# Kernel tuning notes

Measured on AMD Instinct MI355X. Metric: run time of the kernel, lower is better.

## Reference

```python
import jax, jax.numpy as jnp
import numpy as np

DIM = 768
HEADS = 12
HEAD_DIM = DIM // HEADS
SCALE = HEAD_DIM ** -0.5
BATCH = 4      # B videos
FRAMES = 64    # f frames
NTOK = 128     # W_TP tokens per window


def setup_inputs() -> dict:
    key = jax.random.key(0)
    ks = jax.random.split(key, 6)
    x = jax.random.normal(ks[0], (BATCH * FRAMES, NTOK, DIM), jnp.float32)
    # binary mask per frame (zeros are later masked_fill'd to -10000)
    mask = (jax.random.uniform(ks[1], (FRAMES, NTOK, NTOK)) > 0.2).astype(jnp.float32)
    edge_bias = jax.random.normal(ks[2], (NTOK, NTOK), jnp.float32)
    qkv_w = jax.random.normal(ks[3], (3 * DIM, DIM), jnp.float32) * (DIM ** -0.5)
    qkv_b = jnp.zeros((3 * DIM,), jnp.float32)
    proj_w = jax.random.normal(ks[4], (DIM, DIM), jnp.float32) * (DIM ** -0.5)
    proj_b = jnp.zeros((DIM,), jnp.float32)
    return {"x": x, "mask": mask, "edge_bias": edge_bias,
            "qkv_w": qkv_w, "qkv_b": qkv_b,
            "proj_w": proj_w, "proj_b": proj_b,
            "B": BATCH, "f": FRAMES}


def reference(x, mask, edge_bias, qkv_w, qkv_b, proj_w, proj_b, B, f):
    B_f, N, D = x.shape
    H, Dh = HEADS, D // HEADS
    # qkv projection -> [3, B_f, H, N, Dh]
    qkv = (x @ qkv_w.T + qkv_b).reshape(B_f, N, 3, H, Dh)
    qkv = jnp.transpose(qkv, (2, 0, 3, 1, 4))
    q = qkv[0] * jnp.float32(SCALE)
    k = qkv[1]
    v = qkv[2]
    # raw scores [B_f, H, N, N]
    attn = jnp.einsum('bhnd,bhmd->bhnm', q, k)
    # mask multiply ([1,f,1,N,N]) and edge-bias multiply ([1,1,1,N,N])
    attn = attn.reshape(B, f, H, N, N)
    attn = attn * mask[None, :, None] * edge_bias[None, None, None]
    attn = attn.reshape(B_f, H, N, N)
    # masked_fill(attn == 0, -10000) then softmax of NEGATED scores
    attn = jnp.where(attn == 0.0, jnp.float32(-10000.0), attn)
    attn = jax.nn.softmax(-attn, axis=-1)
    out = jnp.einsum('bhnm,bhmd->bhnd', attn, v)  # [B_f,H,N,Dh]
    out = jnp.transpose(out, (0, 2, 1, 3)).reshape(B_f, N, D)
    return out @ proj_w.T + proj_b
```

## Files before the change

kernel.cpp:

```cpp
#include <hip/hip_runtime.h>

typedef unsigned short u16;
typedef unsigned int   u32;
typedef unsigned long long u64;

typedef __attribute__((ext_vector_type(8))) short bf16x8;
typedef __attribute__((ext_vector_type(4))) float f32x4;
typedef __attribute__((ext_vector_type(4))) unsigned int u32x4;

__device__ __forceinline__ u16 rne_bf16(float f) {
  u32 u = __builtin_bit_cast(u32, f);
  u = (u + 0x7fffu + ((u >> 16) & 1u)) >> 16;
  return (u16)u;
}
__device__ __forceinline__ u32 pack_bf16x2(float lo, float hi) {
  return (u32)rne_bf16(lo) | ((u32)rne_bf16(hi) << 16);
}
__device__ __forceinline__ u32 cvt_pk_bf16(float lo, float hi) {
  u32 r;
  asm volatile("v_cvt_pk_bf16_f32 %0, %1, %2" : "=v"(r) : "v"(lo), "v"(hi));
  return r;
}

__global__ __launch_bounds__(256)
void prep_small(const float* __restrict__ mask,
                const float* __restrict__ proj_w, const float* __restrict__ qkv_b,
                const float* __restrict__ proj_b,
                u64* __restrict__ bm0, u64* __restrict__ bm1,
                float* __restrict__ invc, float* __restrict__ cbias) {
  const int b = blockIdx.x;
  const int lane = threadIdx.x & 63;
  if (b < 2048) {
    int row = b * 4 + (threadIdx.x >> 6);
    float v0 = mask[(long)row * 128 + lane];
    float v1 = mask[(long)row * 128 + 64 + lane];
    u64 b0 = __ballot(v0 == 0.0f);
    u64 b1 = __ballot(v1 == 0.0f);
    if (lane == 0) {
      bm0[row] = b0; bm1[row] = b1;
      int c = __builtin_popcountll(b0) + __builtin_popcountll(b1);
      invc[row] = c ? (1.0f / (float)c) : 0.0f;
    }
  } else {
    int i = (b - 2048) * 4 + (threadIdx.x >> 6);
    float s = 0.f;
    for (int j = lane; j < 768; j += 64) s += proj_w[(long)i * 768 + j] * qkv_b[1536 + j];
    #pragma unroll
    for (int off = 32; off; off >>= 1) s += __shfl_down(s, off);
    if (lane == 0) cbias[i] = s + proj_b[i];
  }
}

__global__ __launch_bounds__(256)
void transpose_wv(const float* __restrict__ qkv_w, u16* __restrict__ WvT) {
  __shared__ float tile[64][65];
  int tj = blockIdx.x % 12, td = blockIdx.x / 12;
  int t = threadIdx.x;
  const float* src = qkv_w + (long)1536 * 768 + (long)(tj * 64) * 768 + td * 64;
  #pragma unroll
  for (int i = 0; i < 4; ++i) {
    int j = (t >> 4) + 16 * i;
    int d = (t & 15) * 4;
    float4 v = *(const float4*)&src[(long)j * 768 + d];
    tile[j][d] = v.x; tile[j][d + 1] = v.y; tile[j][d + 2] = v.z; tile[j][d + 3] = v.w;
  }
  __syncthreads();
  u16* dst = WvT + (long)(td * 64) * 768 + tj * 64;
  #pragma unroll
  for (int i = 0; i < 4; ++i) {
    int d = (t >> 4) + 16 * i;
    int j = (t & 15) * 4;
    uint2 p;
    p.x = pack_bf16x2(tile[j][d],     tile[j + 1][d]);
    p.y = pack_bf16x2(tile[j + 2][d], tile[j + 3][d]);
    *(uint2*)&dst[(long)d * 768 + j] = p;
  }
}

template<bool A_FP32, bool B_FP32, bool BF16_OUT>
__global__ __launch_bounds__(256, 4)
void gemm_bt(const void* __restrict__ Av, const void* __restrict__ Bv,
             void* __restrict__ Cv, const float* __restrict__ bias,
             int M, int N, int K, int nblk) {
  __shared__ u16 lA[2][128 * 32];
  __shared__ u16 lB[2][128 * 32];

  const int nwg = gridDim.x;
  const int bid = blockIdx.x;
  const int qq = nwg >> 3, rr8 = nwg & 7;
  const int xcd = bid & 7, loc = bid >> 3;
  const int swz = (xcd < rr8) ? (xcd * (qq + 1) + loc)
                              : (rr8 * (qq + 1) + (xcd - rr8) * qq + loc);
  const int mb = swz / nblk, nb = swz % nblk;
  const long arow0 = (long)mb * 128;
  const long brow0 = (long)nb * 128;

  const int tid = threadIdx.x;
  const int lane = tid & 63, wid = tid >> 6;
  const int wr = wid >> 1, wc = wid & 1;

  const int nk = K >> 5;

  f32x4 acc[4][4];
  const f32x4 vzero = {0.f, 0.f, 0.f, 0.f};
  #pragma unroll
  for (int i = 0; i < 4; ++i)
    #pragma unroll
    for (int j = 0; j < 4; ++j) acc[i][j] = vzero;

  auto stage = [&](int buf, int kt) {
    if constexpr (B_FP32) {
      const float* Bf = (const float*)Bv;
      #pragma unroll
      for (int i = 0; i < 4; ++i) {
        int row = 32 * i + (tid >> 3);
        int kk = 4 * (tid & 7);
        float4 v = *(const float4*)&Bf[(brow0 + row) * (long)K + kt * 32 + kk];
        uint2 p; p.x = pack_bf16x2(v.x, v.y); p.y = pack_bf16x2(v.z, v.w);
        int byte = row * 64 + ((8 * (tid & 7)) ^ (((row >> 1) & 3) << 4));
        *(uint2*)((char*)&lB[buf][0] + byte) = p;
      }
    } else {
      const u16* Bb = (const u16*)Bv;
      #pragma unroll
      for (int i = 0; i < 2; ++i) {
        int tt = tid + 256 * i;
        int gsrc = (tt & 3) ^ ((tt >> 3) & 3);
        const u16* g = &Bb[(brow0 + (tt >> 2)) * (long)K + kt * 32 + 8 * gsrc];
        __builtin_amdgcn_global_load_lds(
            static_cast<const u32*>(static_cast<const void*>(g)),
            static_cast<u32*>(static_cast<void*>(&lB[buf][512 * wid + 2048 * i])),
            16, 0, 0);
      }
    }
    if constexpr (A_FP32) {
      const float* Af = (const float*)Av;
      #pragma unroll
      for (int i = 0; i < 4; ++i) {
        int row = 32 * i + (tid >> 3);
        int kk = 4 * (tid & 7);
        float4 v = *(const float4*)&Af[(arow0 + row) * (long)K + kt * 32 + kk];
        uint2 p; p.x = pack_bf16x2(v.x, v.y); p.y = pack_bf16x2(v.z, v.w);
        int byte = row * 64 + ((8 * (tid & 7)) ^ (((row >> 1) & 3) << 4));
        *(uint2*)((char*)&lA[buf][0] + byte) = p;
      }
    } else {
      const u16* Ab = (const u16*)Av;
      #pragma unroll
      for (int i = 0; i < 2; ++i) {
        int tt = tid + 256 * i;
        int gsrc = (tt & 3) ^ ((tt >> 3) & 3);
        const u16* g = &Ab[(arow0 + (tt >> 2)) * (long)K + kt * 32 + 8 * gsrc];
        __builtin_amdgcn_global_load_lds(
            static_cast<const u32*>(static_cast<const void*>(g)),
            static_cast<u32*>(static_cast<void*>(&lA[buf][512 * wid + 2048 * i])),
            16, 0, 0);
      }
    }
  };

  stage(0, 0);
  __syncthreads();

  int cur = 0;
  for (int kt = 0; kt < nk; ++kt) {
    if (kt + 1 < nk) stage(cur ^ 1, kt + 1);
    bf16x8 afr[4], bfr[4];
    #pragma unroll
    for (int i = 0; i < 4; ++i) {
      int ra = 64 * wr + 16 * i + (lane & 15);
      afr[i] = *(const bf16x8*)((const char*)&lA[cur][0] +
                ra * 64 + ((16 * (lane >> 4)) ^ (((ra >> 1) & 3) << 4)));
      int rb = 64 * wc + 16 * i + (lane & 15);
      bfr[i] = *(const bf16x8*)((const char*)&lB[cur][0] +
                rb * 64 + ((16 * (lane >> 4)) ^ (((rb >> 1) & 3) << 4)));
    }
    #pragma unroll
    for (int b = 0; b < 4; ++b)
      #pragma unroll
      for (int a = 0; a < 4; ++a)
        acc[b][a] = __builtin_amdgcn_mfma_f32_16x16x32_bf16(bfr[b], afr[a], acc[b][a], 0, 0, 0);
    __syncthreads();
    cur ^= 1;
  }

  #pragma unroll
  for (int b = 0; b < 4; ++b) {
    long n0 = brow0 + 64 * wc + 16 * b + 4 * (lane >> 4);
    #pragma unroll
    for (int a = 0; a < 4; ++a) {
      long m = arow0 + 64 * wr + 16 * a + (lane & 15);
      if constexpr (BF16_OUT) {
        uint2 p;
        p.x = pack_bf16x2(acc[b][a][0], acc[b][a][1]);
        p.y = pack_bf16x2(acc[b][a][2], acc[b][a][3]);
        *(uint2*)&((u16*)Cv)[m * N + n0] = p;
      } else {
        const float4 bb = *(const float4*)&bias[n0];
        float4 o;
        o.x = acc[b][a][0] + bb.x; o.y = acc[b][a][1] + bb.y;
        o.z = acc[b][a][2] + bb.z; o.w = acc[b][a][3] + bb.w;
        *(float4*)&((float*)Cv)[m * N + n0] = o;
      }
    }
  }
}

__global__ __launch_bounds__(256, 3)
void msa_fused(const u16* __restrict__ Wc, const float* __restrict__ x,
               const u64* __restrict__ bm0, const u64* __restrict__ bm1,
               const float* __restrict__ invc, const float* __restrict__ cbias,
               float* __restrict__ out) {
  __shared__ alignas(16) char smem[51200];
  u16*   lA  = (u16*)smem;
  char*  lBf = smem + 16384;
  u64*   lbm = (u64*)(smem + 49152);
  u16*   lYT = (u16*)smem;

  const int bid = blockIdx.x;
  const int swz = (bid & 7) * 192 + (bid >> 3);
  const int bfi  = swz / 6;
  const int iblk = swz - 6 * bfi;
  const int fr   = bfi & 63;
  const long arow0 = (long)iblk * 128;
  const long brow0 = (long)bfi * 128;

  const int tid = threadIdx.x;
  const int lane = tid & 63, wid = tid >> 6;
  const int wr = wid >> 1, wc = wid & 1;

  if (tid < 128) {
    lbm[2 * tid]     = bm0[fr * 128 + tid];
    lbm[2 * tid + 1] = bm1[fr * 128 + tid];
  }

  f32x4 acc[4][4];
  const f32x4 vzero = {0.f, 0.f, 0.f, 0.f};
  #pragma unroll
  for (int i = 0; i < 4; ++i)
    #pragma unroll
    for (int j = 0; j < 4; ++j) acc[i][j] = vzero;

  auto stage = [&](int buf, int kt) {
    #pragma unroll
    for (int i = 0; i < 2; ++i) {
      int tt = tid + 256 * i;
      int gsrc = (tt & 3) ^ ((tt >> 3) & 3);
      const u16* g = &Wc[(arow0 + (tt >> 2)) * 768 + kt * 32 + 8 * gsrc];
      __builtin_amdgcn_global_load_lds(
          static_cast<const u32*>(static_cast<const void*>(g)),
          static_cast<u32*>(static_cast<void*>(lA + buf * 4096 + 512 * wid + 2048 * i)),
          16, 0, 0);
    }
    #pragma unroll
    for (int i = 0; i < 4; ++i) {
      int G = i * 256 + tid;
      int r = G >> 3;
      int gl = (G & 7) ^ (r & 7);
      const float* g = &x[(brow0 + r) * 768L + kt * 32 + 4 * gl];
      __builtin_amdgcn_global_load_lds(
          static_cast<const u32*>(static_cast<const void*>(g)),
          static_cast<u32*>(static_cast<void*>(lBf + buf * 16384 + i * 4096 + wid * 1024 + lane * 16)),
          16, 0, 0);
    }
  };

  stage(0, 0);
  __syncthreads();

  int cur = 0;
  for (int kt = 0; kt < 24; ++kt) {
    if (kt + 1 < 24) stage(cur ^ 1, kt + 1);
    bf16x8 afr[4], bfr[4];
    #pragma unroll
    for (int i = 0; i < 4; ++i) {
      int ra = 64 * wr + 16 * i + (lane & 15);
      afr[i] = *(const bf16x8*)((const char*)(lA + cur * 4096) +
                ra * 64 + ((16 * (lane >> 4)) ^ (((ra >> 1) & 3) << 4)));
      int t = 64 * wc + 16 * i + (lane & 15);
      const char* base = lBf + cur * 16384 + t * 128;
      int gl0 = 2 * (lane >> 4);
      f32x4 lo = *(const f32x4*)(base + 16 * (gl0 ^ (t & 7)));
      f32x4 hi = *(const f32x4*)(base + 16 * ((gl0 + 1) ^ (t & 7)));
      u32x4 wv;
      wv.x = cvt_pk_bf16(lo[0], lo[1]);
      wv.y = cvt_pk_bf16(lo[2], lo[3]);
      wv.z = cvt_pk_bf16(hi[0], hi[1]);
      wv.w = cvt_pk_bf16(hi[2], hi[3]);
      bfr[i] = __builtin_bit_cast(bf16x8, wv);
    }
    #pragma unroll
    for (int b = 0; b < 4; ++b)
      #pragma unroll
      for (int a = 0; a < 4; ++a)
        acc[b][a] = __builtin_amdgcn_mfma_f32_16x16x32_bf16(bfr[b], afr[a], acc[b][a], 0, 0, 0);
    __syncthreads();
    cur ^= 1;
  }

  #pragma unroll
  for (int b = 0; b < 4; ++b) {
    int mq = 64 * wc + 16 * b + 4 * (lane >> 4);
    #pragma unroll
    for (int a = 0; a < 4; ++a) {
      int i = 64 * wr + 16 * a + (lane & 15);
      uint2 p;
      p.x = pack_bf16x2(acc[b][a][0], acc[b][a][1]);
      p.y = pack_bf16x2(acc[b][a][2], acc[b][a][3]);
      int sw = (i & 15) ^ ((i >> 4) & 3);
      int byte = i * 256 + (((mq >> 3) ^ sw) << 4) + (mq & 7) * 2;
      *(uint2*)((char*)lYT + byte) = p;
    }
  }
  __syncthreads();

  f32x4 acc2[4][4];
  #pragma unroll
  for (int i = 0; i < 4; ++i)
    #pragma unroll
    for (int j = 0; j < 4; ++j) acc2[i][j] = vzero;

  const unsigned char* lbmB = (const unsigned char*)lbm;
  #pragma unroll
  for (int kk = 0; kk < 4; ++kk) {
    int klog = 64 * kk + 16 * (lane >> 4);
    bf16x8 yfr[4], mfr[4];
    #pragma unroll
    for (int ii = 0; ii < 4; ++ii) {
      int i = 64 * wr + 16 * ii + (lane & 15);
      int sw = ((i & 15) ^ ((i >> 4) & 3)) << 4;
      yfr[ii] = *(const bf16x8*)((char*)lYT + i * 256 + (klog ^ sw));
    }
    #pragma unroll
    for (int tt = 0; tt < 4; ++tt) {
      int t = 64 * wc + 16 * tt + (lane & 15);
      u32 b8 = lbmB[t * 16 + 4 * kk + (lane >> 4)];
      u32x4 wv;
      wv.x = ((b8 & 1)  ? 0x3f80u : 0u) | ((b8 & 2)   ? 0x3f800000u : 0u);
      wv.y = ((b8 & 4)  ? 0x3f80u : 0u) | ((b8 & 8)   ? 0x3f800000u : 0u);
      wv.z = ((b8 & 16) ? 0x3f80u : 0u) | ((b8 & 32)  ? 0x3f800000u : 0u);
      wv.w = ((b8 & 64) ? 0x3f80u : 0u) | ((b8 & 128) ? 0x3f800000u : 0u);
      mfr[tt] = __builtin_bit_cast(bf16x8, wv);
    }
    #pragma unroll
    for (int ii = 0; ii < 4; ++ii)
      #pragma unroll
      for (int tt = 0; tt < 4; ++tt)
        acc2[ii][tt] = __builtin_amdgcn_mfma_f32_16x16x32_bf16(yfr[ii], mfr[tt], acc2[ii][tt], 0, 0, 0);
  }

  const float* icp = invc + fr * 128;
  float icv[4];
  #pragma unroll
  for (int tt = 0; tt < 4; ++tt) icv[tt] = icp[64 * wc + 16 * tt + (lane & 15)];
  #pragma unroll
  for (int ii = 0; ii < 4; ++ii) {
    int i0 = iblk * 128 + 64 * wr + 16 * ii + 4 * (lane >> 4);
    float4 cb4 = *(const float4*)&cbias[i0];
    #pragma unroll
    for (int tt = 0; tt < 4; ++tt) {
      long tok = brow0 + 64 * wc + 16 * tt + (lane & 15);
      float4 o;
      o.x = acc2[ii][tt][0] * icv[tt] + cb4.x;
      o.y = acc2[ii][tt][1] * icv[tt] + cb4.y;
      o.z = acc2[ii][tt][2] * icv[tt] + cb4.z;
      o.w = acc2[ii][tt][3] * icv[tt] + cb4.w;
      *(float4*)&out[tok * 768 + i0] = o;
    }
  }
}

extern "C" void kernel_launch(void* const* d_in, const int* in_sizes, int n_in,
                              void* d_out, int out_size, void* d_ws, size_t ws_size,
                              hipStream_t stream) {
  (void)in_sizes; (void)n_in; (void)out_size; (void)ws_size;
  const float* x      = (const float*)d_in[0];
  const float* mask   = (const float*)d_in[1];
  const float* qkv_w  = (const float*)d_in[3];
  const float* qkv_b  = (const float*)d_in[4];
  const float* proj_w = (const float*)d_in[5];
  const float* proj_b = (const float*)d_in[6];

  char* w = (char*)d_ws;
  u16*   WvT  = (u16*)(w);
  u16*   Wc   = (u16*)(w + 0x120000);
  float* cb   = (float*)(w + 0x240000);
  u64*   bm0  = (u64*)(w + 0x241000);
  u64*   bm1  = (u64*)(w + 0x251000);
  float* invc = (float*)(w + 0x261000);

  prep_small<<<dim3(2240), dim3(256), 0, stream>>>(mask, proj_w, qkv_b, proj_b,
                                                   bm0, bm1, invc, cb);
  transpose_wv<<<dim3(144), dim3(256), 0, stream>>>(qkv_w, WvT);
  gemm_bt<true, false, true><<<dim3(36), dim3(256), 0, stream>>>(
      (const void*)proj_w, (const void*)WvT, (void*)Wc, nullptr, 768, 768, 768, 6);
  msa_fused<<<dim3(1536), dim3(256), 0, stream>>>(Wc, x, bm0, bm1, invc, cb, (float*)d_out);
}
```

Before: 110.1 us.

## Load weight fragments directly from global and shrink LDS for higher occupancy

The weight (A) operand is no longer staged through LDS; each lane reads its bf16x8 fragment straight from global memory every k-step. Only the fp32 x tile is double-buffered in LDS, now in a two-half layout with a new XOR swizzle. LDS use falls from 50 KB to 34 KB and launch bounds rise to 4 blocks per CU, aiming for more occupancy. In exchange, the A loads now sit on the critical path without prefetch, and register pressure rises under the tighter launch bound.

New measurement: 142.6 us. 1.3x slower.

```diff
diff --git a/kernel.cpp b/kernel.cpp
--- a/kernel.cpp
+++ b/kernel.cpp
@@ -206,15 +206,14 @@
   }
 }
 
-__global__ __launch_bounds__(256, 3)
+__global__ __launch_bounds__(256, 4)
 void msa_fused(const u16* __restrict__ Wc, const float* __restrict__ x,
                const u64* __restrict__ bm0, const u64* __restrict__ bm1,
                const float* __restrict__ invc, const float* __restrict__ cbias,
                float* __restrict__ out) {
-  __shared__ alignas(16) char smem[51200];
-  u16*   lA  = (u16*)smem;
-  char*  lBf = smem + 16384;
-  u64*   lbm = (u64*)(smem + 49152);
+  __shared__ alignas(16) char smem[34816];
+  char*  lBf = smem;
+  u64*   lbm = (u64*)(smem + 32768);
   u16*   lYT = (u16*)smem;
 
   const int bid = blockIdx.x;
@@ -241,23 +240,13 @@
     #pragma unroll
     for (int j = 0; j < 4; ++j) acc[i][j] = vzero;
 
-  auto stage = [&](int buf, int kt) {
-    #pragma unroll
-    for (int i = 0; i < 2; ++i) {
-      int tt = tid + 256 * i;
-      int gsrc = (tt & 3) ^ ((tt >> 3) & 3);
-      const u16* g = &Wc[(arow0 + (tt >> 2)) * 768 + kt * 32 + 8 * gsrc];
-      __builtin_amdgcn_global_load_lds(
-          static_cast<const u32*>(static_cast<const void*>(g)),
-          static_cast<u32*>(static_cast<void*>(lA + buf * 4096 + 512 * wid + 2048 * i)),
-          16, 0, 0);
-    }
+  auto stageB = [&](int buf, int kt) {
     #pragma unroll
     for (int i = 0; i < 4; ++i) {
       int G = i * 256 + tid;
-      int r = G >> 3;
-      int gl = (G & 7) ^ (r & 7);
-      const float* g = &x[(brow0 + r) * 768L + kt * 32 + 4 * gl];
+      int h = G >> 9, r = (G >> 2) & 127, gp = G & 3;
+      int gl = gp ^ ((r >> 1) & 3);
+      const float* g = &x[(brow0 + r) * 768L + kt * 32 + h * 16 + 4 * gl];
       __builtin_amdgcn_global_load_lds(
           static_cast<const u32*>(static_cast<const void*>(g)),
           static_cast<u32*>(static_cast<void*>(lBf + buf * 16384 + i * 4096 + wid * 1024 + lane * 16)),
@@ -265,23 +254,26 @@
     }
   };
 
-  stage(0, 0);
+  stageB(0, 0);
   __syncthreads();
 
+  const int q = lane >> 4, qh = q >> 1, ql = q & 1;
   int cur = 0;
   for (int kt = 0; kt < 24; ++kt) {
-    if (kt + 1 < 24) stage(cur ^ 1, kt + 1);
+    if (kt + 1 < 24) stageB(cur ^ 1, kt + 1);
     bf16x8 afr[4], bfr[4];
     #pragma unroll
     for (int i = 0; i < 4; ++i) {
       int ra = 64 * wr + 16 * i + (lane & 15);
-      afr[i] = *(const bf16x8*)((const char*)(lA + cur * 4096) +
-                ra * 64 + ((16 * (lane >> 4)) ^ (((ra >> 1) & 3) << 4)));
+      afr[i] = *(const bf16x8*)&Wc[(arow0 + ra) * 768L + kt * 32 + 8 * q];
+    }
+    #pragma unroll
+    for (int i = 0; i < 4; ++i) {
       int t = 64 * wc + 16 * i + (lane & 15);
-      const char* base = lBf + cur * 16384 + t * 128;
-      int gl0 = 2 * (lane >> 4);
-      f32x4 lo = *(const f32x4*)(base + 16 * (gl0 ^ (t & 7)));
-      f32x4 hi = *(const f32x4*)(base + 16 * ((gl0 + 1) ^ (t & 7)));
+      const char* base = lBf + cur * 16384 + qh * 8192 + t * 64;
+      int sw = (t >> 1) & 3;
+      f32x4 lo = *(const f32x4*)(base + 16 * ((2 * ql) ^ sw));
+      f32x4 hi = *(const f32x4*)(base + 16 * ((2 * ql + 1) ^ sw));
       u32x4 wv;
       wv.x = cvt_pk_bf16(lo[0], lo[1]);
       wv.y = cvt_pk_bf16(lo[2], lo[3]);
```
